# Kernel optimization log

Measured on AMD Instinct MI355X. Metric: run time of the kernel, lower is better.

The kernel has to match this reference:

```python
import jax, jax.numpy as jnp
import numpy as np

T, B, I = 1000, 16, 440   # time, batch, input feat
H, P = 1024, 512          # cell size, projection size


def setup_inputs() -> dict:
    key = jax.random.key(0)
    ks = jax.random.split(key, 14)
    s_in = 1.0 / np.sqrt(I)
    s_p = 1.0 / np.sqrt(P)
    s_h = 1.0 / np.sqrt(H)
    inp = {
        "x": jax.random.normal(ks[0], (T, B, I), jnp.float32),
        # input->gate linears (bias=True since no batchnorm/laynorm)
        "wfx_w": jax.random.uniform(ks[1], (H, I), jnp.float32, -s_in, s_in),
        "wfx_b": jax.random.uniform(ks[2], (H,), jnp.float32, -s_in, s_in),
        "wix_w": jax.random.uniform(ks[3], (H, I), jnp.float32, -s_in, s_in),
        "wix_b": jax.random.uniform(ks[4], (H,), jnp.float32, -s_in, s_in),
        "wox_w": jax.random.uniform(ks[5], (H, I), jnp.float32, -s_in, s_in),
        "wox_b": jax.random.uniform(ks[6], (H,), jnp.float32, -s_in, s_in),
        "wcx_w": jax.random.uniform(ks[7], (H, I), jnp.float32, -s_in, s_in),
        "wcx_b": jax.random.uniform(ks[8], (H,), jnp.float32, -s_in, s_in),
        # recurrent projections (bias=False)
        "tfy_w": jax.random.uniform(ks[9], (H, P), jnp.float32, -s_p, s_p),
        "tiy_w": jax.random.uniform(ks[10], (H, P), jnp.float32, -s_p, s_p),
        "toy_w": jax.random.uniform(ks[11], (H, P), jnp.float32, -s_p, s_p),
        "tcy_w": jax.random.uniform(ks[12], (H, P), jnp.float32, -s_p, s_p),
        # output projection h -> y (bias=False)
        "wym_w": jax.random.uniform(ks[13], (P, H), jnp.float32, -s_h, s_h),
    }
    return inp


def reference(x, wfx_w, wfx_b, wix_w, wix_b, wox_w, wox_b, wcx_w, wcx_b,
              tfy_w, tiy_w, toy_w, tcy_w, wym_w):
    # Precompute input-to-gate projections for all timesteps: [T,B,H]
    gf = jnp.einsum('tbi,hi->tbh', x, wfx_w) + wfx_b
    gi = jnp.einsum('tbi,hi->tbh', x, wix_w) + wix_b
    go = jnp.einsum('tbi,hi->tbh', x, wox_w) + wox_b
    gc = jnp.einsum('tbi,hi->tbh', x, wcx_w) + wcx_b

    b = x.shape[1]
    c0 = jnp.zeros((b, H), x.dtype)  # h_init in source (used as cell state)
    y0 = jnp.zeros((b, P), x.dtype)
    drop_mask = jnp.asarray(1.0, x.dtype)  # test mode: 1 - drop, drop=0.0

    def step(carry, g):
        ct, yt = carry
        gf_t, gi_t, go_t, gc_t = g
        it = jax.nn.sigmoid(gi_t + yt @ tiy_w.T)
        ft = jax.nn.sigmoid(gf_t + yt @ tfy_w.T)
        ot = jax.nn.sigmoid(go_t + yt @ toy_w.T)
        ct = it * jnp.tanh(gc_t + yt @ tcy_w.T) * drop_mask + ft * ct
        ht = ot * jnp.tanh(ct)
        yt = ht @ wym_w.T
        return (ct, yt), ht

    _, h = jax.lax.scan(step, (c0, y0), (gf, gi, go, gc))
    return h  # [T, B, H]
```

## Files before the change

kernel.cpp:

```cpp
#include <hip/hip_runtime.h>
#include <hip/hip_fp16.h>
#include <stdint.h>

#define T_STEPS 1000
#define BATCH   16
#define IFEAT   440
#define KPAD    448
#define HDIM    1024
#define PDIM    512
#define NWG     64

typedef _Float16 f16x8 __attribute__((ext_vector_type(8)));
typedef _Float16 f16x4 __attribute__((ext_vector_type(4)));
typedef float    f32x4 __attribute__((ext_vector_type(4)));
typedef uint32_t u32x4 __attribute__((ext_vector_type(4)));

union F16x8U { f16x8 v; u32x4 w; };

#define OFF_HB    0u
#define OFF_XH    65536u
#define OFF_W4    (OFF_XH + 14336000u)
#define OFF_TG    (OFF_W4 + 3670016u)
#define OFF_WYT   (OFF_TG + 4194304u)
#define OFF_M     (OFF_WYT + 1048576u)
#define OFF_GX    (OFF_M + 8388608u)

__device__ __forceinline__ float sigm_(float x)  { return 1.f / (1.f + __expf(-x)); }
__device__ __forceinline__ float tanh_(float x)  { return 1.f - 2.f / (1.f + __expf(2.f * x)); }

__global__ void init_hb(unsigned short* __restrict__ HB) {
    int i = blockIdx.x * 256 + threadIdx.x;
    HB[i] = (i < BATCH * HDIM) ? (unsigned short)0x0000 : (unsigned short)0x0001;
}

__global__ void prep_x(const float* __restrict__ x, _Float16* __restrict__ xh) {
    int idx = blockIdx.x * 256 + threadIdx.x;
    const int total = T_STEPS * BATCH * KPAD;
    for (; idx < total; idx += gridDim.x * 256) {
        int k = idx % KPAD;
        int row = idx / KPAD;
        float v = (k < IFEAT) ? x[row * IFEAT + k] : 0.f;
        xh[idx] = (_Float16)v;
    }
}

__global__ void prep_w(const float* __restrict__ wi, const float* __restrict__ wf,
                       const float* __restrict__ wo, const float* __restrict__ wc,
                       const float* __restrict__ ti, const float* __restrict__ tf,
                       const float* __restrict__ to_, const float* __restrict__ tc,
                       const float* __restrict__ wym,
                       _Float16* __restrict__ W4, _Float16* __restrict__ TG,
                       _Float16* __restrict__ WYT) {
    int tid = blockIdx.x * 256 + threadIdx.x;
    int stride = gridDim.x * 256;
    const float* const Wsrc[4] = {wi, wf, wo, wc};
    const float* const Tsrc[4] = {ti, tf, to_, tc};
    const int totW = 4 * HDIM * KPAD;
    for (int idx = tid; idx < totW; idx += stride) {
        int k = idx % KPAD; int gh = idx / KPAD;
        int h = gh % HDIM;  int g = gh / HDIM;
        W4[idx] = (_Float16)((k < IFEAT) ? Wsrc[g][h * IFEAT + k] : 0.f);
    }
    const int totT = 4 * HDIM * PDIM;
    for (int idx = tid; idx < totT; idx += stride) {
        int p = idx % PDIM; int gh = idx / PDIM;
        int h = gh % HDIM;  int g = gh / HDIM;
        TG[idx] = (_Float16)Tsrc[g][h * PDIM + p];
    }
    const int totY = HDIM * PDIM;
    for (int idx = tid; idx < totY; idx += stride) {
        int p = idx % PDIM; int hh = idx / PDIM;
        WYT[idx] = (_Float16)wym[p * HDIM + hh];
    }
}

__global__ __launch_bounds__(256) void mgemm(const _Float16* __restrict__ TG,
                                             const _Float16* __restrict__ WYT,
                                             _Float16* __restrict__ M) {
    int wave = threadIdx.x >> 6, l = threadIdx.x & 63;
    int lo = l & 15, quad = l >> 4;
    int tile = blockIdx.x * 4 + wave;
    int g = tile >> 12;
    int ht = (tile >> 6) & 63;
    int hht = tile & 63;
    const _Float16* Ar = TG  + ((size_t)(g * HDIM + ht * 16 + lo)) * PDIM;
    const _Float16* Br = WYT + ((size_t)(hht * 16 + lo)) * PDIM;
    f32x4 acc = {0.f, 0.f, 0.f, 0.f};
#pragma unroll
    for (int cc = 0; cc < 16; ++cc) {
        f16x8 a = *(const f16x8*)(Ar + cc * 32 + quad * 8);
        f16x8 b = *(const f16x8*)(Br + cc * 32 + quad * 8);
        acc = __builtin_amdgcn_mfma_f32_16x16x32_f16(a, b, acc, 0, 0, 0);
    }
    _Float16* dst = M + (size_t)g * HDIM * HDIM;
#pragma unroll
    for (int r = 0; r < 4; ++r)
        dst[(size_t)(ht * 16 + quad * 4 + r) * HDIM + hht * 16 + lo] = (_Float16)acc[r];
}

#define TT 4
__global__ __launch_bounds__(256) void phase1(const _Float16* __restrict__ xh,
                                              const _Float16* __restrict__ W4,
                                              const float* __restrict__ bI,
                                              const float* __restrict__ bF,
                                              const float* __restrict__ bO,
                                              const float* __restrict__ bC,
                                              _Float16* __restrict__ GX) {
    __shared__ _Float16 sx[TT * 16 * 456];
    const int t0 = blockIdx.x * TT;
    for (int c = threadIdx.x; c < TT * 16 * 56; c += 256) {
        int kc = c % 56, rowi = c / 56;
        *(f16x8*)(sx + rowi * 456 + kc * 8) =
            *(const f16x8*)(xh + ((size_t)(t0 * 16 + rowi)) * KPAD + kc * 8);
    }
    __syncthreads();
    const int wave = threadIdx.x >> 6, l = threadIdx.x & 63;
    const int lo = l & 15, quad = l >> 4;
    const int g = wave;
    const float* bias = (g == 0) ? bI : (g == 1) ? bF : (g == 2) ? bO : bC;
    for (int htp = 0; htp < 32; ++htp) {
        const int ht0 = htp * 2, ht1 = htp * 2 + 1;
        f16x8 A0[14], A1[14];
        const _Float16* Ar0 = W4 + ((size_t)(g * HDIM + ht0 * 16 + lo)) * KPAD;
        const _Float16* Ar1 = Ar0 + (size_t)16 * KPAD;
#pragma unroll
        for (int cc = 0; cc < 14; ++cc) {
            A0[cc] = *(const f16x8*)(Ar0 + cc * 32 + quad * 8);
            A1[cc] = *(const f16x8*)(Ar1 + cc * 32 + quad * 8);
        }
        float b0[4], b1[4];
#pragma unroll
        for (int r = 0; r < 4; ++r) {
            b0[r] = bias[ht0 * 16 + quad * 4 + r];
            b1[r] = bias[ht1 * 16 + quad * 4 + r];
        }
        for (int t = 0; t < TT; ++t) {
            f32x4 acc0 = {0.f, 0.f, 0.f, 0.f}, acc1 = {0.f, 0.f, 0.f, 0.f};
#pragma unroll
            for (int cc = 0; cc < 14; ++cc) {
                f16x8 b = *(const f16x8*)(sx + (t * 16 + lo) * 456 + cc * 32 + quad * 8);
                acc0 = __builtin_amdgcn_mfma_f32_16x16x32_f16(A0[cc], b, acc0, 0, 0, 0);
                acc1 = __builtin_amdgcn_mfma_f32_16x16x32_f16(A1[cc], b, acc1, 0, 0, 0);
            }
            size_t tbase = ((size_t)(t0 + t) * 4 + g) * 64;
            f16x4 h0, h1;
#pragma unroll
            for (int r = 0; r < 4; ++r) {
                h0[r] = (_Float16)(acc0[r] + b0[r]);
                h1[r] = (_Float16)(acc1[r] + b1[r]);
            }
            *(f16x4*)(GX + ((tbase + ht0) * 64 + l) * 4) = h0;
            *(f16x4*)(GX + ((tbase + ht1) * 64 + l) * 4) = h1;
        }
    }
}

__global__ __launch_bounds__(320, 1) void recur(const _Float16* __restrict__ GX,
                                                const _Float16* __restrict__ Mw,
                                                _Float16* __restrict__ HB,
                                                float* __restrict__ out) {
    const int tid = threadIdx.x, wave = tid >> 6, l = tid & 63;
    const int lo = l & 15, quad = l >> 4;
    const int ht = blockIdx.x;

    __shared__ float P[2][4][4][64][4];
    __shared__ f16x4 GXR[4][4][64];
    __shared__ f32x4 OUTB[64];
    __shared__ int hvstep_s;
    __shared__ int gxready_s;

    if (tid == 0) hvstep_s = -1;

    if (wave < 4) {
        const int kbase = wave * 256;

        f16x8 A[4][8];
#pragma unroll
        for (int g = 0; g < 4; ++g) {
            const _Float16* Ar = Mw + ((size_t)g * HDIM + ht * 16 + lo) * HDIM + kbase;
#pragma unroll
            for (int cc = 0; cc < 8; ++cc)
                A[g][cc] = *(const f16x8*)(Ar + cc * 32 + quad * 8);
        }

        f32x4 ct = {0.f, 0.f, 0.f, 0.f};
        const _Float16* hb0 = HB + (size_t)lo * HDIM + kbase + quad * 8;
        _Float16* hs0 = HB + (size_t)lo * HDIM + ht * 16 + quad * 4;

        __syncthreads();

        for (int t = 0; t < T_STEPS; ++t) {
            const int par = t & 1;
            const uint32_t expw = ((t >> 1) & 1) ? 0x00010001u : 0u;
            const uint64_t pollA = (uint64_t)(uintptr_t)(hb0 + (size_t)par * BATCH * HDIM);

            F16x8U B[8];
            while (true) {
                asm volatile(
                    "global_load_dwordx4 %0, %8, off sc0 sc1\n\t"
                    "global_load_dwordx4 %1, %8, off offset:64 sc0 sc1\n\t"
                    "global_load_dwordx4 %2, %8, off offset:128 sc0 sc1\n\t"
                    "global_load_dwordx4 %3, %8, off offset:192 sc0 sc1\n\t"
                    "global_load_dwordx4 %4, %8, off offset:256 sc0 sc1\n\t"
                    "global_load_dwordx4 %5, %8, off offset:320 sc0 sc1\n\t"
                    "global_load_dwordx4 %6, %8, off offset:384 sc0 sc1\n\t"
                    "global_load_dwordx4 %7, %8, off offset:448 sc0 sc1\n\t"
                    "s_waitcnt vmcnt(0)"
                    : "=&v"(B[0].w), "=&v"(B[1].w), "=&v"(B[2].w), "=&v"(B[3].w),
                      "=&v"(B[4].w), "=&v"(B[5].w), "=&v"(B[6].w), "=&v"(B[7].w)
                    : "v"(pollA)
                    : "memory");
                uint32_t bad = 0;
#pragma unroll
                for (int c = 0; c < 8; ++c)
#pragma unroll
                    for (int j = 0; j < 4; ++j)
                        bad |= (B[c].w[j] ^ expw) & 0x00010001u;
                if (__all(bad == 0)) break;
            }

            f32x4 acc[4];
#pragma unroll
            for (int g = 0; g < 4; ++g) acc[g] = (f32x4){0.f, 0.f, 0.f, 0.f};
#pragma unroll
            for (int cc = 0; cc < 8; ++cc) {
#pragma unroll
                for (int g = 0; g < 4; ++g)
                    acc[g] = __builtin_amdgcn_mfma_f32_16x16x32_f16(A[g][cc], B[cc].v, acc[g], 0, 0, 0);
            }
#pragma unroll
            for (int g = 0; g < 4; ++g)
                *(f32x4*)&P[par][wave][g][l][0] = acc[g];

            __syncthreads();

            if (wave == 0) {
                f32x4 pre[4];
#pragma unroll
                for (int g = 0; g < 4; ++g) {
                    f32x4 s = *(const f32x4*)&P[par][0][g][l][0];
#pragma unroll
                    for (int k = 1; k < 4; ++k) s = s + *(const f32x4*)&P[par][k][g][l][0];
                    pre[g] = s;
                }
                while (__hip_atomic_load(&gxready_s, __ATOMIC_ACQUIRE,
                                         __HIP_MEMORY_SCOPE_WORKGROUP) < t)
                    __builtin_amdgcn_s_sleep(1);
#pragma unroll
                for (int g = 0; g < 4; ++g) {
                    f16x4 gv = GXR[t & 3][g][l];
#pragma unroll
                    for (int r = 0; r < 4; ++r) pre[g][r] += (float)gv[r];
                }
                f32x4 hv; f16x4 hh;
#pragma unroll
                for (int r = 0; r < 4; ++r) {
                    float it = sigm_(pre[0][r]);
                    float ft = sigm_(pre[1][r]);
                    float ot = sigm_(pre[2][r]);
                    float gt = tanh_(pre[3][r]);
                    ct[r] = it * gt + ft * ct[r];
                    float h = ot * tanh_(ct[r]);
                    hv[r] = h; hh[r] = (_Float16)h;
                }
                unsigned long long bits; __builtin_memcpy(&bits, &hh, 8);
                const unsigned long long TAG = 0x0001000100010001ULL;
                unsigned long long genw = (unsigned long long)(((t + 1) >> 1) & 1);
                bits = (bits & ~TAG) | (genw * TAG);
                uint64_t sA = (uint64_t)(uintptr_t)(hs0 + (size_t)((t + 1) & 1) * BATCH * HDIM);
                asm volatile("global_store_dwordx2 %0, %1, off sc0 sc1"
                             :: "v"(sA), "v"(bits) : "memory");
                OUTB[l] = hv;
                if (l == 0)
                    __hip_atomic_store(&hvstep_s, t, __ATOMIC_RELEASE,
                                       __HIP_MEMORY_SCOPE_WORKGROUP);
            }
        }
    } else {
        f16x4 G[4];
#pragma unroll
        for (int s = 0; s < 2; ++s)
#pragma unroll
            for (int g = 0; g < 4; ++g)
                GXR[s][g][l] = *(const f16x4*)(GX + ((((size_t)s * 4 + g) * 64 + ht) * 64 + l) * 4);
#pragma unroll
        for (int g = 0; g < 4; ++g)
            G[g] = *(const f16x4*)(GX + ((((size_t)2 * 4 + g) * 64 + ht) * 64 + l) * 4);
        if (l == 0)
            __hip_atomic_store(&gxready_s, 1, __ATOMIC_RELEASE,
                               __HIP_MEMORY_SCOPE_WORKGROUP);
        __syncthreads();

        for (int t = 0; t < T_STEPS; ++t) {
            __syncthreads();
            while (__hip_atomic_load(&hvstep_s, __ATOMIC_ACQUIRE,
                                     __HIP_MEMORY_SCOPE_WORKGROUP) < t)
                __builtin_amdgcn_s_sleep(1);
#pragma unroll
            for (int g = 0; g < 4; ++g) GXR[(t + 2) & 3][g][l] = G[g];
            if (l == 0)
                __hip_atomic_store(&gxready_s, t + 2, __ATOMIC_RELEASE,
                                   __HIP_MEMORY_SCOPE_WORKGROUP);
            f32x4 hv = OUTB[l];
            __builtin_nontemporal_store(hv,
                (f32x4*)(out + ((size_t)t * BATCH + lo) * HDIM + ht * 16 + quad * 4));
            int tp = (t + 3 < T_STEPS) ? (t + 3) : (T_STEPS - 1);
#pragma unroll
            for (int g = 0; g < 4; ++g)
                G[g] = *(const f16x4*)(GX + ((((size_t)tp * 4 + g) * 64 + ht) * 64 + l) * 4);
        }
    }
}

extern "C" void kernel_launch(void* const* d_in, const int* in_sizes, int n_in,
                              void* d_out, int out_size, void* d_ws, size_t ws_size,
                              hipStream_t stream) {
    const float* x    = (const float*)d_in[0];
    const float* wfxw = (const float*)d_in[1];
    const float* wfxb = (const float*)d_in[2];
    const float* wixw = (const float*)d_in[3];
    const float* wixb = (const float*)d_in[4];
    const float* woxw = (const float*)d_in[5];
    const float* woxb = (const float*)d_in[6];
    const float* wcxw = (const float*)d_in[7];
    const float* wcxb = (const float*)d_in[8];
    const float* tfyw = (const float*)d_in[9];
    const float* tiyw = (const float*)d_in[10];
    const float* toyw = (const float*)d_in[11];
    const float* tcyw = (const float*)d_in[12];
    const float* wymw = (const float*)d_in[13];

    char* ws = (char*)d_ws;
    _Float16*  HB    = (_Float16*)(ws + OFF_HB);
    _Float16*  XH    = (_Float16*)(ws + OFF_XH);
    _Float16*  W4    = (_Float16*)(ws + OFF_W4);
    _Float16*  TG    = (_Float16*)(ws + OFF_TG);
    _Float16*  WYT   = (_Float16*)(ws + OFF_WYT);
    _Float16*  Mw    = (_Float16*)(ws + OFF_M);
    _Float16*  GX    = (_Float16*)(ws + OFF_GX);
    float* out = (float*)d_out;

    init_hb<<<128, 256, 0, stream>>>((unsigned short*)HB);
    prep_x<<<4096, 256, 0, stream>>>(x, XH);
    prep_w<<<2048, 256, 0, stream>>>(wixw, wfxw, woxw, wcxw,
                                     tiyw, tfyw, toyw, tcyw, wymw,
                                     W4, TG, WYT);
    mgemm<<<4096, 256, 0, stream>>>(TG, WYT, Mw);
    phase1<<<250, 256, 0, stream>>>(XH, W4, wixb, wfxb, woxb, wcxb, GX);
    recur<<<NWG, 320, 0, stream>>>(GX, Mw, HB, out);
}
```

Measured before the change: 4.593 ms.

## Replace tag-bit polling on hidden-state buffer with per-workgroup step flags

Cross-workgroup synchronization no longer embeds generation tag bits in the fp16 hidden state and re-polls the full 8x16B vector loads. Each workgroup now publishes a step counter flag after storing its hidden slice, and consumers poll a single dword flag per lane before loading the state once. This keeps the low mantissa bit intact and cuts polling traffic, but adds a store-wait plus an extra flag store on the critical path. The flags reuse the XH region, which is safe only because phase1 has already consumed XH. A spin limit breaks out after many iterations.

```diff
diff --git a/kernel.cpp b/kernel.cpp
--- a/kernel.cpp
+++ b/kernel.cpp
@@ -30,7 +30,11 @@
 
 __global__ void init_hb(unsigned short* __restrict__ HB) {
     int i = blockIdx.x * 256 + threadIdx.x;
-    HB[i] = (i < BATCH * HDIM) ? (unsigned short)0x0000 : (unsigned short)0x0001;
+    HB[i] = 0;
+}
+
+__global__ void init_sync(int* __restrict__ S) {
+    if (threadIdx.x < 64) S[threadIdx.x] = 0;
 }
 
 __global__ void prep_x(const float* __restrict__ x, _Float16* __restrict__ xh) {
@@ -158,7 +162,8 @@
 __global__ __launch_bounds__(320, 1) void recur(const _Float16* __restrict__ GX,
                                                 const _Float16* __restrict__ Mw,
                                                 _Float16* __restrict__ HB,
-                                                float* __restrict__ out) {
+                                                float* __restrict__ out,
+                                                int* __restrict__ FLAGS) {
     const int tid = threadIdx.x, wave = tid >> 6, l = tid & 63;
     const int lo = l & 15, quad = l >> 4;
     const int ht = blockIdx.x;
@@ -186,38 +191,40 @@
         f32x4 ct = {0.f, 0.f, 0.f, 0.f};
         const _Float16* hb0 = HB + (size_t)lo * HDIM + kbase + quad * 8;
         _Float16* hs0 = HB + (size_t)lo * HDIM + ht * 16 + quad * 4;
+        const uint64_t fA = (uint64_t)(uintptr_t)(FLAGS + wave * 16 + (l & 15));
+        const uint64_t fsA = (uint64_t)(uintptr_t)(FLAGS + ht);
 
         __syncthreads();
 
         for (int t = 0; t < T_STEPS; ++t) {
             const int par = t & 1;
-            const uint32_t expw = ((t >> 1) & 1) ? 0x00010001u : 0u;
-            const uint64_t pollA = (uint64_t)(uintptr_t)(hb0 + (size_t)par * BATCH * HDIM);
-
+
+            if (t > 0) {
+                int f, spins = 0;
+                do {
+                    asm volatile("global_load_dword %0, %1, off sc0 sc1\n\t"
+                                 "s_waitcnt vmcnt(0)"
+                                 : "=v"(f) : "v"(fA) : "memory");
+                    if (++spins > (1 << 20)) break;
+                } while (!__all(f >= t));
+            }
+
+            const uint64_t bA = (uint64_t)(uintptr_t)(hb0 + (size_t)par * BATCH * HDIM);
             F16x8U B[8];
-            while (true) {
-                asm volatile(
-                    "global_load_dwordx4 %0, %8, off sc0 sc1\n\t"
-                    "global_load_dwordx4 %1, %8, off offset:64 sc0 sc1\n\t"
-                    "global_load_dwordx4 %2, %8, off offset:128 sc0 sc1\n\t"
-                    "global_load_dwordx4 %3, %8, off offset:192 sc0 sc1\n\t"
-                    "global_load_dwordx4 %4, %8, off offset:256 sc0 sc1\n\t"
-                    "global_load_dwordx4 %5, %8, off offset:320 sc0 sc1\n\t"
-                    "global_load_dwordx4 %6, %8, off offset:384 sc0 sc1\n\t"
-                    "global_load_dwordx4 %7, %8, off offset:448 sc0 sc1\n\t"
-                    "s_waitcnt vmcnt(0)"
-                    : "=&v"(B[0].w), "=&v"(B[1].w), "=&v"(B[2].w), "=&v"(B[3].w),
-                      "=&v"(B[4].w), "=&v"(B[5].w), "=&v"(B[6].w), "=&v"(B[7].w)
-                    : "v"(pollA)
-                    : "memory");
-                uint32_t bad = 0;
-#pragma unroll
-                for (int c = 0; c < 8; ++c)
-#pragma unroll
-                    for (int j = 0; j < 4; ++j)
-                        bad |= (B[c].w[j] ^ expw) & 0x00010001u;
-                if (__all(bad == 0)) break;
-            }
+            asm volatile(
+                "global_load_dwordx4 %0, %8, off sc0 sc1\n\t"
+                "global_load_dwordx4 %1, %8, off offset:64 sc0 sc1\n\t"
+                "global_load_dwordx4 %2, %8, off offset:128 sc0 sc1\n\t"
+                "global_load_dwordx4 %3, %8, off offset:192 sc0 sc1\n\t"
+                "global_load_dwordx4 %4, %8, off offset:256 sc0 sc1\n\t"
+                "global_load_dwordx4 %5, %8, off offset:320 sc0 sc1\n\t"
+                "global_load_dwordx4 %6, %8, off offset:384 sc0 sc1\n\t"
+                "global_load_dwordx4 %7, %8, off offset:448 sc0 sc1\n\t"
+                "s_waitcnt vmcnt(0)"
+                : "=&v"(B[0].w), "=&v"(B[1].w), "=&v"(B[2].w), "=&v"(B[3].w),
+                  "=&v"(B[4].w), "=&v"(B[5].w), "=&v"(B[6].w), "=&v"(B[7].w)
+                : "v"(bA)
+                : "memory");
 
             f32x4 acc[4];
 #pragma unroll
@@ -264,12 +271,15 @@
                     hv[r] = h; hh[r] = (_Float16)h;
                 }
                 unsigned long long bits; __builtin_memcpy(&bits, &hh, 8);
-                const unsigned long long TAG = 0x0001000100010001ULL;
-                unsigned long long genw = (unsigned long long)(((t + 1) >> 1) & 1);
-                bits = (bits & ~TAG) | (genw * TAG);
-                uint64_t sA = (uint64_t)(uintptr_t)(hs0 + (size_t)((t + 1) & 1) * BATCH * HDIM);
+                const uint64_t sA = (uint64_t)(uintptr_t)(hs0 + (size_t)((t + 1) & 1) * BATCH * HDIM);
                 asm volatile("global_store_dwordx2 %0, %1, off sc0 sc1"
                              :: "v"(sA), "v"(bits) : "memory");
+                asm volatile("s_waitcnt vmcnt(0)" ::: "memory");
+                if (l == 0) {
+                    int gen = t + 1;
+                    asm volatile("global_store_dword %0, %1, off sc0 sc1"
+                                 :: "v"(fsA), "v"(gen) : "memory");
+                }
                 OUTB[l] = hv;
                 if (l == 0)
                     __hip_atomic_store(&hvstep_s, t, __ATOMIC_RELEASE,
@@ -333,6 +343,7 @@
     char* ws = (char*)d_ws;
     _Float16*  HB    = (_Float16*)(ws + OFF_HB);
     _Float16*  XH    = (_Float16*)(ws + OFF_XH);
+    int*       FLAGS = (int*)(ws + OFF_XH);
     _Float16*  W4    = (_Float16*)(ws + OFF_W4);
     _Float16*  TG    = (_Float16*)(ws + OFF_TG);
     _Float16*  WYT   = (_Float16*)(ws + OFF_WYT);
@@ -347,5 +358,6 @@
                                      W4, TG, WYT);
     mgemm<<<4096, 256, 0, stream>>>(TG, WYT, Mw);
     phase1<<<250, 256, 0, stream>>>(XH, W4, wixb, wfxb, woxb, wcxb, GX);
-    recur<<<NWG, 320, 0, stream>>>(GX, Mw, HB, out);
-}
+    init_sync<<<1, 64, 0, stream>>>(FLAGS);
+    recur<<<NWG, 320, 0, stream>>>(GX, Mw, HB, out, FLAGS);
+}
```

After: 5.183 ms. +12.8%, slower.
